# Kernel tuning notes

Hardware: AMD Instinct MI355X
Metric: run time of the kernel (lower is better)

## Reference

```python
import jax, jax.numpy as jnp
import numpy as np

B, DZ, H, DY = 4096, 512, 2048, 10
N_STEPS = 64
SCALE = 0.02  # matches param_ulow/uhigh magnitude


def setup_inputs() -> dict:
    key = jax.random.key(0)
    ks = jax.random.split(key, 6)
    x = jax.random.normal(ks[0], (B, DZ), dtype=jnp.float32)
    A = jax.random.normal(ks[1], (DZ, DZ), dtype=jnp.float32) * SCALE
    W1 = jax.random.normal(ks[2], (H, DZ), dtype=jnp.float32) * SCALE
    b1 = jax.random.normal(ks[3], (H,), dtype=jnp.float32) * SCALE
    W2 = jax.random.normal(ks[4], (DY, H), dtype=jnp.float32) * SCALE
    b2 = jax.random.normal(ks[5], (DY,), dtype=jnp.float32) * SCALE
    return {"x": x, "A": A, "W1": W1, "b1": b1, "W2": W2, "b2": b2,
            "n_steps": N_STEPS}


def reference(x, A, W1, b1, W2, b2, n_steps):
    # Z0 = P @ x with P = I  => Z0 = x
    # dz/dt = einsum('ji,bi->bj', A, z) = z @ A.T ; explicit Euler on [0, 1]
    dt = jnp.float32(1.0 / n_steps)

    def euler_step(z, _):
        return z + dt * (z @ A.T), None

    zT, _ = jax.lax.scan(euler_step, x, None, length=n_steps)  # [B, DZ]
    # Q MLP (n_layers=3): Linear -> ReLU -> Linear
    h = jax.nn.relu(zT @ W1.T + b1)  # [B, H]
    y = h @ W2.T + b2                # [B, DY]
    return y
```

## Files before the change

kernel.cpp:

```cpp
#include <hip/hip_runtime.h>
#include <hip/hip_bf16.h>

#define B_SZ 4096
#define DZ   512
#define H_SZ 2048
#define DY   10

#define C2 0.4921875f
#define C3 0.158935546875f
#define C4 0.037872314453125f
#define C5 ((float)(7624512.0/1073741824.0))
#define C6 ((float)(74974368.0/68719476736.0))

typedef __attribute__((ext_vector_type(8))) __bf16 bf16x8;
typedef __attribute__((ext_vector_type(4))) float  f32x4;
typedef __attribute__((ext_vector_type(8))) unsigned short us8;

__device__ inline unsigned short f2bf(float f) {
    unsigned u = __float_as_uint(f);
    u += 0x7fffu + ((u >> 16) & 1u);
    return (unsigned short)(u >> 16);
}
__device__ inline float bf2f(unsigned short s) {
    return __uint_as_float(((unsigned)s) << 16);
}

__device__ __forceinline__ void gl16(const void* g, void* l) {
    __builtin_amdgcn_global_load_lds(
        (const __attribute__((address_space(1))) unsigned int*)(size_t)g,
        (__attribute__((address_space(3))) unsigned int*)(unsigned)(size_t)l,
        16, 0, 0);
}

union SqSmem {
    struct { unsigned short A[64 * 64]; unsigned short B[64 * 64]; } s;
    float epi[64 * 68];
};

__device__ __forceinline__ void stage64(const unsigned short* __restrict__ src,
                                        unsigned short* lds, int row_base,
                                        int kt, int t) {
    const int w = t >> 6, lane = t & 63;
#pragma unroll
    for (int i = 0; i < 2; ++i) {
        int o = w * 128 + i * 64 + lane;
        int row = o >> 3, cc = (o & 7) ^ (row & 7);
        gl16(&src[(size_t)(row_base + row) * 512 + kt * 64 + cc * 8],
             &lds[(size_t)(w * 128 + i * 64) * 8]);
    }
}

#define MFMA_STEP(acc)                                                        \
    {                                                                         \
        _Pragma("unroll")                                                     \
        for (int ks = 0; ks < 2; ++ks) {                                      \
            bf16x8 af[2], bfr[2];                                             \
            _Pragma("unroll")                                                 \
            for (int i = 0; i < 2; ++i) {                                     \
                int ra = wm + i * 16 + l16, ca = (ks * 4 + quad) ^ (ra & 7);  \
                af[i] = *(const bf16x8*)&sm.s.A[ra * 64 + ca * 8];            \
                int rb = wn + i * 16 + l16, cb = (ks * 4 + quad) ^ (rb & 7);  \
                bfr[i] = *(const bf16x8*)&sm.s.B[rb * 64 + cb * 8];           \
            }                                                                 \
            _Pragma("unroll")                                                 \
            for (int i = 0; i < 2; ++i)                                       \
                _Pragma("unroll")                                             \
                for (int j = 0; j < 2; ++j)                                   \
                    acc[i][j] = __builtin_amdgcn_mfma_f32_16x16x32_bf16(      \
                        af[i], bfr[j], acc[i][j], 0, 0, 0);                   \
        }                                                                     \
    }

#define ACC_TO_EPI(acc)                                                       \
    {                                                                         \
        _Pragma("unroll")                                                     \
        for (int i = 0; i < 2; ++i)                                           \
            _Pragma("unroll")                                                 \
            for (int j = 0; j < 2; ++j)                                       \
                _Pragma("unroll")                                             \
                for (int rr = 0; rr < 4; ++rr)                                \
                    sm.epi[(wm + i * 16 + quad * 4 + rr) * 68 +               \
                           wn + j * 16 + l16] = acc[i][j][rr];                \
        __syncthreads();                                                      \
    }

__device__ inline void gemm64_mfma(const unsigned short* __restrict__ Arows,
                                   const unsigned short* __restrict__ Brows,
                                   int m0, int n0, int t, SqSmem& sm) {
    const int lane = t & 63, w = t >> 6, quad = lane >> 4, l16 = lane & 15;
    const int wm = (w & 1) * 32, wn = (w >> 1) * 32;
    f32x4 acc[2][2];
#pragma unroll
    for (int i = 0; i < 2; ++i)
#pragma unroll
        for (int j = 0; j < 2; ++j) acc[i][j] = (f32x4){0.f, 0.f, 0.f, 0.f};
    for (int kt = 0; kt < 8; ++kt) {
        stage64(Arows, sm.s.A, m0, kt, t);
        stage64(Brows, sm.s.B, n0, kt, t);
        __syncthreads();
        MFMA_STEP(acc)
        __syncthreads();
    }
    ACC_TO_EPI(acc)
}

__device__ inline void gemm64_f32src(const float* __restrict__ Arows,
                                     const float* __restrict__ Bsrc,
                                     int m0, int n0, int t, SqSmem& sm) {
    const int lane = t & 63, w = t >> 6, quad = lane >> 4, l16 = lane & 15;
    const int wm = (w & 1) * 32, wn = (w >> 1) * 32;
    const int r = t >> 2, cq = t & 3;
    f32x4 acc[2][2];
#pragma unroll
    for (int i = 0; i < 2; ++i)
#pragma unroll
        for (int j = 0; j < 2; ++j) acc[i][j] = (f32x4){0.f, 0.f, 0.f, 0.f};
    for (int kt = 0; kt < 8; ++kt) {
        float va[16];
#pragma unroll
        for (int u = 0; u < 4; ++u) {
            float4 f = *(const float4*)&Arows[(size_t)(m0 + r) * 512 + kt * 64 + cq * 16 + u * 4];
            va[u * 4 + 0] = f.x; va[u * 4 + 1] = f.y;
            va[u * 4 + 2] = f.z; va[u * 4 + 3] = f.w;
        }
#pragma unroll
        for (int j2 = 0; j2 < 2; ++j2) {
            us8 h;
#pragma unroll
            for (int j = 0; j < 8; ++j) h[j] = f2bf(va[j2 * 8 + j]);
            int cc = cq * 2 + j2;
            *(us8*)&sm.s.A[r * 64 + (cc ^ (r & 7)) * 8] = h;
        }
#pragma unroll
        for (int u = 0; u < 4; ++u) {
            float4 f = *(const float4*)&Bsrc[(size_t)(kt * 64 + r) * 512 + n0 + cq * 16 + u * 4];
            float vv[4] = {f.x, f.y, f.z, f.w};
#pragma unroll
            for (int j = 0; j < 4; ++j) {
                int n = cq * 16 + u * 4 + j;
                sm.s.B[n * 64 + ((r >> 3) ^ (n & 7)) * 8 + (r & 7)] = f2bf(vv[j]);
            }
        }
        __syncthreads();
        MFMA_STEP(acc)
        __syncthreads();
    }
    ACC_TO_EPI(acc)
}

__device__ inline void epi_out_bf(unsigned short* __restrict__ dst, int m0,
                                  int n0, int t, SqSmem& sm) {
    const int r = t >> 2, cq = t & 3;
    us8 h0, h1;
#pragma unroll
    for (int j = 0; j < 8; ++j) {
        h0[j] = f2bf(sm.epi[r * 68 + cq * 16 + j]);
        h1[j] = f2bf(sm.epi[r * 68 + cq * 16 + 8 + j]);
    }
    *(us8*)&dst[(size_t)(m0 + r) * 512 + n0 + cq * 16]     = h0;
    *(us8*)&dst[(size_t)(m0 + r) * 512 + n0 + cq * 16 + 8] = h1;
}
__device__ inline void epi_out_bfT(unsigned short* __restrict__ dst, int m0,
                                   int n0, int t, SqSmem& sm) {
    const int cf = t >> 2, rq = t & 3;
    us8 o0, o1;
#pragma unroll
    for (int i = 0; i < 8; ++i) {
        o0[i] = f2bf(sm.epi[(rq * 16 + i) * 68 + cf]);
        o1[i] = f2bf(sm.epi[(rq * 16 + 8 + i) * 68 + cf]);
    }
    *(us8*)&dst[(size_t)(n0 + cf) * 512 + m0 + rq * 16]     = o0;
    *(us8*)&dst[(size_t)(n0 + cf) * 512 + m0 + rq * 16 + 8] = o1;
}

__global__ __launch_bounds__(256) void k_s1(
    const float* __restrict__ A, const float* __restrict__ x,
    const float* __restrict__ W1, const float* __restrict__ b2,
    unsigned short* __restrict__ A2_bf, unsigned short* __restrict__ A2T_bf,
    unsigned short* __restrict__ AT_bf, unsigned short* __restrict__ U1_bf,
    unsigned short* __restrict__ x_bf, float* __restrict__ y) {
    __shared__ SqSmem sm;
    const int b = blockIdx.x, t = threadIdx.x;
    const int gid = b * 256 + t;

    const float4* x4 = (const float4*)x;
#pragma unroll
    for (int i = 0; i < 3; ++i) {
        int id = gid + i * 98304;
        if (id < 262144) {
            float4 v0 = x4[(size_t)id * 2], v1 = x4[(size_t)id * 2 + 1];
            us8 o;
            o[0] = f2bf(v0.x); o[1] = f2bf(v0.y); o[2] = f2bf(v0.z); o[3] = f2bf(v0.w);
            o[4] = f2bf(v1.x); o[5] = f2bf(v1.y); o[6] = f2bf(v1.z); o[7] = f2bf(v1.w);
            *(us8*)&x_bf[(size_t)id * 8] = o;
        }
    }
    if (gid < B_SZ * DY) y[gid] = b2[gid % 10];

    if (b < 64) {
        const int m0 = (b >> 3) * 64, n0 = (b & 7) * 64;
        gemm64_f32src(A, A, m0, n0, t, sm);
        epi_out_bf(A2_bf, m0, n0, t, sm);
        epi_out_bfT(A2T_bf, m0, n0, t, sm);
    } else if (b < 128) {
        const int bb = b - 64, m0 = (bb >> 3) * 64, n0 = (bb & 7) * 64;
        const int r = t >> 2, cq = t & 3;
#pragma unroll
        for (int u = 0; u < 4; ++u) {
            float4 f = *(const float4*)&A[(size_t)(m0 + r) * 512 + n0 + cq * 16 + u * 4];
            sm.epi[r * 68 + cq * 16 + u * 4 + 0] = f.x;
            sm.epi[r * 68 + cq * 16 + u * 4 + 1] = f.y;
            sm.epi[r * 68 + cq * 16 + u * 4 + 2] = f.z;
            sm.epi[r * 68 + cq * 16 + u * 4 + 3] = f.w;
        }
        __syncthreads();
        epi_out_bfT(AT_bf, m0, n0, t, sm);
    } else {
        const int bb = b - 128, m0 = (bb >> 3) * 64, n0 = (bb & 7) * 64;
        gemm64_f32src(W1, A, m0, n0, t, sm);
        epi_out_bf(U1_bf, m0, n0, t, sm);
    }
}

__global__ __launch_bounds__(256) void k_s2(
    const unsigned short* __restrict__ A2_bf,
    const unsigned short* __restrict__ A2T_bf,
    const unsigned short* __restrict__ AT_bf,
    const unsigned short* __restrict__ U1_bf,
    unsigned short* __restrict__ A3T_bf, unsigned short* __restrict__ U2_bf,
    unsigned short* __restrict__ U3_bf) {
    __shared__ SqSmem sm;
    const int b = blockIdx.x, t = threadIdx.x;
    if (b < 64) {
        const int m0 = (b >> 3) * 64, n0 = (b & 7) * 64;
        gemm64_mfma(A2_bf, AT_bf, m0, n0, t, sm);
        epi_out_bfT(A3T_bf, m0, n0, t, sm);
    } else if (b < 320) {
        const int bb = b - 64, m0 = (bb >> 3) * 64, n0 = (bb & 7) * 64;
        gemm64_mfma(U1_bf, AT_bf, m0, n0, t, sm);
        epi_out_bf(U2_bf, m0, n0, t, sm);
    } else {
        const int bb = b - 320, m0 = (bb >> 3) * 64, n0 = (bb & 7) * 64;
        gemm64_mfma(U1_bf, A2T_bf, m0, n0, t, sm);
        epi_out_bf(U3_bf, m0, n0, t, sm);
    }
}

__global__ __launch_bounds__(256) void k_s3(
    const float* __restrict__ W1, const unsigned short* __restrict__ U1_bf,
    const unsigned short* __restrict__ U2_bf,
    const unsigned short* __restrict__ U3_bf,
    const unsigned short* __restrict__ A3T_bf,
    unsigned short* __restrict__ w1f) {
    __shared__ SqSmem sm;
    const int b = blockIdx.x, t = threadIdx.x;
    const int m0 = (b >> 3) * 64, n0 = (b & 7) * 64;
    const int lane = t & 63, w = t >> 6, quad = lane >> 4, l16 = lane & 15;
    const int wm = (w & 1) * 32, wn = (w >> 1) * 32;
    f32x4 acc[2][2];
#pragma unroll
    for (int i = 0; i < 2; ++i)
#pragma unroll
        for (int j = 0; j < 2; ++j) acc[i][j] = (f32x4){0.f, 0.f, 0.f, 0.f};
    for (int kt = 0; kt < 8; ++kt) {
        stage64(A3T_bf, sm.s.B, n0, kt, t);
#pragma unroll
        for (int c = 0; c < 2; ++c) {
            int idx = c * 256 + t, row = idx >> 3, cc = idx & 7;
            int ccs = cc ^ (row & 7);
            size_t ga = (size_t)(m0 + row) * 512 + kt * 64 + cc * 8;
            us8 u1 = *(const us8*)&U1_bf[ga];
            us8 u2 = *(const us8*)&U2_bf[ga];
            us8 u3 = *(const us8*)&U3_bf[ga];
            us8 g;
#pragma unroll
            for (int j = 0; j < 8; ++j)
                g[j] = f2bf(C4 * bf2f(u1[j]) + C5 * bf2f(u2[j]) + C6 * bf2f(u3[j]));
            *(us8*)&sm.s.A[row * 64 + ccs * 8] = g;
        }
        __syncthreads();
        MFMA_STEP(acc)
        __syncthreads();
    }
    ACC_TO_EPI(acc)
    const int r = t >> 2, cq = t & 3;
    size_t gbase = (size_t)(m0 + r) * 512 + n0 + cq * 16;
    us8 u1a = *(const us8*)&U1_bf[gbase], u1b = *(const us8*)&U1_bf[gbase + 8];
    us8 u2a = *(const us8*)&U2_bf[gbase], u2b = *(const us8*)&U2_bf[gbase + 8];
    us8 u3a = *(const us8*)&U3_bf[gbase], u3b = *(const us8*)&U3_bf[gbase + 8];
    us8 h0, h1;
#pragma unroll
    for (int u = 0; u < 2; ++u) {
        float4 wv = *(const float4*)&W1[gbase + u * 4];
        float4 wv2 = *(const float4*)&W1[gbase + 8 + u * 4];
#pragma unroll
        for (int j = 0; j < 4; ++j) {
            int e = u * 4 + j;
            float wj = (j == 0 ? wv.x : j == 1 ? wv.y : j == 2 ? wv.z : wv.w);
            float wj2 = (j == 0 ? wv2.x : j == 1 ? wv2.y : j == 2 ? wv2.z : wv2.w);
            h0[e] = f2bf(wj + bf2f(u1a[e]) + C2 * bf2f(u2a[e]) +
                         C3 * bf2f(u3a[e]) + sm.epi[r * 68 + cq * 16 + e]);
            h1[e] = f2bf(wj2 + bf2f(u1b[e]) + C2 * bf2f(u2b[e]) +
                         C3 * bf2f(u3b[e]) + sm.epi[r * 68 + cq * 16 + 8 + e]);
        }
    }
    *(us8*)&w1f[gbase]     = h0;
    *(us8*)&w1f[gbase + 8] = h1;
}

union SmemU {
    struct { unsigned short A[128 * 64]; unsigned short B[128 * 64]; } s;
    struct { unsigned short h[128 * 136]; } e;
};

__global__ __launch_bounds__(256) void mlp_kernel(
    const unsigned short* __restrict__ x_bf,
    const unsigned short* __restrict__ w1f,
    const float* __restrict__ b1, const float* __restrict__ W2,
    float* __restrict__ y) {
    __shared__ SmemU sm;
    const int t    = threadIdx.x;
    const int lane = t & 63, w = t >> 6;
    const int quad = lane >> 4, l16 = lane & 15;
    const int wm = (w & 1) * 64, wn = (w >> 1) * 64;
    const int m0g = blockIdx.x * 128, n0g = blockIdx.y * 128;

    f32x4 acc[4][4];
#pragma unroll
    for (int i = 0; i < 4; ++i)
#pragma unroll
        for (int j = 0; j < 4; ++j) acc[i][j] = (f32x4){0.f, 0.f, 0.f, 0.f};

    for (int kt = 0; kt < 8; ++kt) {
#pragma unroll
        for (int i = 0; i < 4; ++i) {
            int o = w * 256 + i * 64 + lane;
            int row = o >> 3, cc = (o & 7) ^ (row & 7);
            gl16(&x_bf[(size_t)(m0g + row) * 512 + kt * 64 + cc * 8],
                 &sm.s.A[(size_t)(w * 256 + i * 64) * 8]);
        }
#pragma unroll
        for (int i = 0; i < 4; ++i) {
            int o = w * 256 + i * 64 + lane;
            int row = o >> 3, cc = (o & 7) ^ (row & 7);
            gl16(&w1f[(size_t)(n0g + row) * 512 + kt * 64 + cc * 8],
                 &sm.s.B[(size_t)(w * 256 + i * 64) * 8]);
        }
        __syncthreads();
#pragma unroll
        for (int ks = 0; ks < 2; ++ks) {
            bf16x8 af[4], bfr[4];
#pragma unroll
            for (int i = 0; i < 4; ++i) {
                int ra = wm + i * 16 + l16, ca = (ks * 4 + quad) ^ (ra & 7);
                af[i] = *(const bf16x8*)&sm.s.A[ra * 64 + ca * 8];
                int rb = wn + i * 16 + l16, cb = (ks * 4 + quad) ^ (rb & 7);
                bfr[i] = *(const bf16x8*)&sm.s.B[rb * 64 + cb * 8];
            }
#pragma unroll
            for (int i = 0; i < 4; ++i)
// ... 23 lines not shown

    {
        bf16x8 wfrag[4];
#pragma unroll
        for (int kc = 0; kc < 4; ++kc) {
            us8 wb;
            if (l16 < DY) {
                const float* wp = &W2[(size_t)l16 * H_SZ + n0g + kc * 32 + quad * 8];
#pragma unroll
                for (int j = 0; j < 8; ++j) wb[j] = f2bf(wp[j]);
            } else {
#pragma unroll
                for (int j = 0; j < 8; ++j) wb[j] = 0;
            }
            wfrag[kc] = *(bf16x8*)&wb;
        }
#pragma unroll
        for (int hh = 0; hh < 2; ++hh) {
            const int mrow = w * 32 + hh * 16;
            f32x4 ay = (f32x4){0.f, 0.f, 0.f, 0.f};
#pragma unroll
            for (int kc = 0; kc < 4; ++kc) {
                bf16x8 af = *(const bf16x8*)&sm.e.h[(mrow + l16) * 136 +
                                                    kc * 32 + quad * 8];
                ay = __builtin_amdgcn_mfma_f32_16x16x32_bf16(af, wfrag[kc], ay,
                                                             0, 0, 0);
            }
            if (l16 < DY) {
#pragma unroll
                for (int r = 0; r < 4; ++r)
                    atomicAdd(&y[(size_t)(m0g + mrow + quad * 4 + r) * DY + l16],
                              ay[r]);
            }
        }
    }
}

extern "C" void kernel_launch(void* const* d_in, const int* in_sizes, int n_in,
                              void* d_out, int out_size, void* d_ws, size_t ws_size,
                              hipStream_t stream) {
    const float* x  = (const float*)d_in[0];
    const float* A  = (const float*)d_in[1];
    const float* W1 = (const float*)d_in[2];
    const float* b1 = (const float*)d_in[3];
    const float* W2 = (const float*)d_in[4];
    const float* b2 = (const float*)d_in[5];
    float* y = (float*)d_out;

    char* ws = (char*)d_ws;
    const size_t HMB = 512u * 1024, MB = 1u << 20;
    unsigned short* AT_bf  = (unsigned short*)(ws);
    unsigned short* A2_bf  = (unsigned short*)(ws + 1 * HMB);
    unsigned short* A2T_bf = (unsigned short*)(ws + 2 * HMB);
    unsigned short* A3T_bf = (unsigned short*)(ws + 3 * HMB);
    unsigned short* U1_bf  = (unsigned short*)(ws + 2 * MB);
    unsigned short* U2_bf  = (unsigned short*)(ws + 4 * MB);
    unsigned short* U3_bf  = (unsigned short*)(ws + 6 * MB);
    unsigned short* w1f    = (unsigned short*)(ws + 8 * MB);
    unsigned short* x_bf   = (unsigned short*)(ws + 10 * MB);

    k_s1<<<384, 256, 0, stream>>>(A, x, W1, b2, A2_bf, A2T_bf, AT_bf, U1_bf,
                                  x_bf, y);
    k_s2<<<576, 256, 0, stream>>>(A2_bf, A2T_bf, AT_bf, U1_bf, A3T_bf, U2_bf,
                                  U3_bf);
    k_s3<<<256, 256, 0, stream>>>(W1, U1_bf, U2_bf, U3_bf, A3T_bf, w1f);
    mlp_kernel<<<dim3(32, 16), dim3(256), 0, stream>>>(x_bf, w1f, b1, W2, y);
}
```

Before: 135.6 us.

## Restructure matrix-power polynomial to use A^3/A^4 and 128-tile GEMMs

After: 171.6 us. 1.27x slower.

```diff
diff --git a/kernel.cpp b/kernel.cpp
--- a/kernel.cpp
+++ b/kernel.cpp
@@ -36,19 +36,6 @@
     struct { unsigned short A[64 * 64]; unsigned short B[64 * 64]; } s;
     float epi[64 * 68];
 };
-
-__device__ __forceinline__ void stage64(const unsigned short* __restrict__ src,
-                                        unsigned short* lds, int row_base,
-                                        int kt, int t) {
-    const int w = t >> 6, lane = t & 63;
-#pragma unroll
-    for (int i = 0; i < 2; ++i) {
-        int o = w * 128 + i * 64 + lane;
-        int row = o >> 3, cc = (o & 7) ^ (row & 7);
-        gl16(&src[(size_t)(row_base + row) * 512 + kt * 64 + cc * 8],
-             &lds[(size_t)(w * 128 + i * 64) * 8]);
-    }
-}
 
 #define MFMA_STEP(acc)                                                        \
     {                                                                         \
@@ -84,26 +71,6 @@
         __syncthreads();                                                      \
     }
 
-__device__ inline void gemm64_mfma(const unsigned short* __restrict__ Arows,
-                                   const unsigned short* __restrict__ Brows,
-                                   int m0, int n0, int t, SqSmem& sm) {
-    const int lane = t & 63, w = t >> 6, quad = lane >> 4, l16 = lane & 15;
-    const int wm = (w & 1) * 32, wn = (w >> 1) * 32;
-    f32x4 acc[2][2];
-#pragma unroll
-    for (int i = 0; i < 2; ++i)
-#pragma unroll
-        for (int j = 0; j < 2; ++j) acc[i][j] = (f32x4){0.f, 0.f, 0.f, 0.f};
-    for (int kt = 0; kt < 8; ++kt) {
-        stage64(Arows, sm.s.A, m0, kt, t);
-        stage64(Brows, sm.s.B, n0, kt, t);
-        __syncthreads();
-        MFMA_STEP(acc)
-        __syncthreads();
-    }
-    ACC_TO_EPI(acc)
-}
-
 __device__ inline void gemm64_f32src(const float* __restrict__ Arows,
                                      const float* __restrict__ Bsrc,
                                      int m0, int n0, int t, SqSmem& sm) {
@@ -173,27 +140,131 @@
     *(us8*)&dst[(size_t)(n0 + cf) * 512 + m0 + rq * 16 + 8] = o1;
 }
 
+union Smem128 {
+    struct { unsigned short A[128 * 64]; unsigned short B[128 * 64]; } s;
+    float epi[128 * 133];
+};
+
+__device__ __forceinline__ void g128_stage(const unsigned short* __restrict__ Asrc,
+                                           const unsigned short* __restrict__ Bsrc,
+                                           int m0, int n0, int kt, int t,
+                                           Smem128& sm) {
+    const int w = t >> 6, lane = t & 63;
+#pragma unroll
+    for (int i = 0; i < 4; ++i) {
+        int o = w * 256 + i * 64 + lane;
+        int row = o >> 3, cc = (o & 7) ^ (row & 7);
+        gl16(&Asrc[(size_t)(m0 + row) * 512 + kt * 64 + cc * 8],
+             &sm.s.A[(w * 256 + i * 64) * 8]);
+        gl16(&Bsrc[(size_t)(n0 + row) * 512 + kt * 64 + cc * 8],
+             &sm.s.B[(w * 256 + i * 64) * 8]);
+    }
+}
+
+__device__ __forceinline__ void g128_mfma(int t, Smem128& sm, f32x4 acc[4][4]) {
+    const int lane = t & 63, w = t >> 6, quad = lane >> 4, l16 = lane & 15;
+    const int wm = (w & 1) * 64, wn = (w >> 1) * 64;
+#pragma unroll
+    for (int ks = 0; ks < 2; ++ks) {
+        bf16x8 af[4], bfr[4];
+#pragma unroll
+        for (int i = 0; i < 4; ++i) {
+            int ra = wm + i * 16 + l16, ca = (ks * 4 + quad) ^ (ra & 7);
+            af[i] = *(const bf16x8*)&sm.s.A[ra * 64 + ca * 8];
+            int rb = wn + i * 16 + l16, cb = (ks * 4 + quad) ^ (rb & 7);
+            bfr[i] = *(const bf16x8*)&sm.s.B[rb * 64 + cb * 8];
+        }
+#pragma unroll
+        for (int i = 0; i < 4; ++i)
+#pragma unroll
+            for (int j = 0; j < 4; ++j)
+                acc[i][j] = __builtin_amdgcn_mfma_f32_16x16x32_bf16(
+                    af[i], bfr[j], acc[i][j], 0, 0, 0);
+    }
+}
+
+__device__ inline void gemm128(const unsigned short* __restrict__ Asrc,
+                               const unsigned short* __restrict__ Bsrc,
+                               int m0, int n0, int t, Smem128& sm,
+                               f32x4 acc[4][4]) {
+    for (int kt = 0; kt < 8; ++kt) {
+        g128_stage(Asrc, Bsrc, m0, n0, kt, t, sm);
+        __syncthreads();
+        g128_mfma(t, sm, acc);
+        __syncthreads();
+    }
+}
+
+__device__ inline void g128_acc2epi(int t, Smem128& sm, f32x4 acc[4][4]) {
+    const int lane = t & 63, w = t >> 6, quad = lane >> 4, l16 = lane & 15;
+    const int wm = (w & 1) * 64, wn = (w >> 1) * 64;
+#pragma unroll
+    for (int i = 0; i < 4; ++i)
+#pragma unroll
+        for (int j = 0; j < 4; ++j)
+#pragma unroll
+            for (int r = 0; r < 4; ++r)
+                sm.epi[(wm + i * 16 + quad * 4 + r) * 133 + wn + j * 16 + l16] =
+                    acc[i][j][r];
+    __syncthreads();
+}
+
+__device__ inline void g128_out(unsigned short* __restrict__ dst, int m0,
+                                int n0, int t, Smem128& sm) {
+    const int r = t >> 1, hf = t & 1;
+    size_t gb = (size_t)(m0 + r) * 512 + n0 + hf * 64;
+#pragma unroll
+    for (int jc = 0; jc < 8; ++jc) {
+        us8 h;
+#pragma unroll
+        for (int j = 0; j < 8; ++j)
+            h[j] = f2bf(sm.epi[r * 133 + hf * 64 + jc * 8 + j]);
+        *(us8*)&dst[gb + jc * 8] = h;
+    }
+}
+__device__ inline void g128_outT(unsigned short* __restrict__ dst, int m0,
+                                 int n0, int t, Smem128& sm) {
+    const int c = t >> 1, hf = t & 1;
+    size_t gb = (size_t)(n0 + c) * 512 + m0 + hf * 64;
+#pragma unroll
+    for (int jc = 0; jc < 8; ++jc) {
+        us8 h;
+#pragma unroll
+        for (int j = 0; j < 8; ++j)
+            h[j] = f2bf(sm.epi[(hf * 64 + jc * 8 + j) * 133 + c]);
+        *(us8*)&dst[gb + jc * 8] = h;
+    }
+}
+
 __global__ __launch_bounds__(256) void k_s1(
     const float* __restrict__ A, const float* __restrict__ x,
     const float* __restrict__ W1, const float* __restrict__ b2,
     unsigned short* __restrict__ A2_bf, unsigned short* __restrict__ A2T_bf,
-    unsigned short* __restrict__ AT_bf, unsigned short* __restrict__ U1_bf,
-    unsigned short* __restrict__ x_bf, float* __restrict__ y) {
+    unsigned short* __restrict__ AT_bf, unsigned short* __restrict__ x_bf,
+    unsigned short* __restrict__ W1_bf, float* __restrict__ y) {
     __shared__ SqSmem sm;
     const int b = blockIdx.x, t = threadIdx.x;
     const int gid = b * 256 + t;
 
     const float4* x4 = (const float4*)x;
 #pragma unroll
-    for (int i = 0; i < 3; ++i) {
-        int id = gid + i * 98304;
-        if (id < 262144) {
-            float4 v0 = x4[(size_t)id * 2], v1 = x4[(size_t)id * 2 + 1];
-            us8 o;
-            o[0] = f2bf(v0.x); o[1] = f2bf(v0.y); o[2] = f2bf(v0.z); o[3] = f2bf(v0.w);
-            o[4] = f2bf(v1.x); o[5] = f2bf(v1.y); o[6] = f2bf(v1.z); o[7] = f2bf(v1.w);
-            *(us8*)&x_bf[(size_t)id * 8] = o;
-        }
+    for (int i = 0; i < 4; ++i) {
+        int id = gid + i * 65536;
+        float4 v0 = x4[(size_t)id * 2], v1 = x4[(size_t)id * 2 + 1];
+        us8 o;
+        o[0] = f2bf(v0.x); o[1] = f2bf(v0.y); o[2] = f2bf(v0.z); o[3] = f2bf(v0.w);
+        o[4] = f2bf(v1.x); o[5] = f2bf(v1.y); o[6] = f2bf(v1.z); o[7] = f2bf(v1.w);
+        *(us8*)&x_bf[(size_t)id * 8] = o;
+    }
+    const float4* w4 = (const float4*)W1;
+#pragma unroll
+    for (int i = 0; i < 2; ++i) {
+        int id = gid + i * 65536;
+        float4 v0 = w4[(size_t)id * 2], v1 = w4[(size_t)id * 2 + 1];
+        us8 o;
+        o[0] = f2bf(v0.x); o[1] = f2bf(v0.y); o[2] = f2bf(v0.z); o[3] = f2bf(v0.w);
+        o[4] = f2bf(v1.x); o[5] = f2bf(v1.y); o[6] = f2bf(v1.z); o[7] = f2bf(v1.w);
+        *(us8*)&W1_bf[(size_t)id * 8] = o;
     }
     if (gid < B_SZ * DY) y[gid] = b2[gid % 10];
 
@@ -215,97 +286,119 @@
         }
         __syncthreads();
         epi_out_bfT(AT_bf, m0, n0, t, sm);
-    } else {
-        const int bb = b - 128, m0 = (bb >> 3) * 64, n0 = (bb & 7) * 64;
-        gemm64_f32src(W1, A, m0, n0, t, sm);
-        epi_out_bf(U1_bf, m0, n0, t, sm);
     }
 }
 
 __global__ __launch_bounds__(256) void k_s2(
+    const unsigned short* __restrict__ W1_bf,
     const unsigned short* __restrict__ A2_bf,
     const unsigned short* __restrict__ A2T_bf,
     const unsigned short* __restrict__ AT_bf,
-    const unsigned short* __restrict__ U1_bf,
-    unsigned short* __restrict__ A3T_bf, unsigned short* __restrict__ U2_bf,
-    unsigned short* __restrict__ U3_bf) {
-    __shared__ SqSmem sm;
+    unsigned short* __restrict__ A3T_bf, unsigned short* __restrict__ A4T_bf,
+    unsigned short* __restrict__ U1_bf, unsigned short* __restrict__ U2_bf) {
+    __shared__ Smem128 sm;
     const int b = blockIdx.x, t = threadIdx.x;
-    if (b < 64) {
-        const int m0 = (b >> 3) * 64, n0 = (b & 7) * 64;
-        gemm64_mfma(A2_bf, AT_bf, m0, n0, t, sm);
-        epi_out_bfT(A3T_bf, m0, n0, t, sm);
-    } else if (b < 320) {
-        const int bb = b - 64, m0 = (bb >> 3) * 64, n0 = (bb & 7) * 64;
-        gemm64_mfma(U1_bf, AT_bf, m0, n0, t, sm);
-        epi_out_bf(U2_bf, m0, n0, t, sm);
+    f32x4 acc[4][4];
+#pragma unroll
+    for (int i = 0; i < 4; ++i)
+#pragma unroll
+        for (int j = 0; j < 4; ++j) acc[i][j] = (f32x4){0.f, 0.f, 0.f, 0.f};
+
+    if (b < 16) {
+        const int m0 = (b >> 2) * 128, n0 = (b & 3) * 128;
+        gemm128(A2_bf, AT_bf, m0, n0, t, sm, acc);
+        g128_acc2epi(t, sm, acc);
+        g128_outT(A3T_bf, m0, n0, t, sm);
+    } else if (b < 32) {
+        const int bb = b - 16, m0 = (bb >> 2) * 128, n0 = (bb & 3) * 128;
+        gemm128(A2_bf, A2T_bf, m0, n0, t, sm, acc);
+        g128_acc2epi(t, sm, acc);
+        g128_outT(A4T_bf, m0, n0, t, sm);
+    } else if (b < 96) {
+        const int bb = b - 32, m0 = (bb >> 2) * 128, n0 = (bb & 3) * 128;
+        gemm128(W1_bf, AT_bf, m0, n0, t, sm, acc);
+        g128_acc2epi(t, sm, acc);
+        g128_out(U1_bf, m0, n0, t, sm);
     } else {
-        const int bb = b - 320, m0 = (bb >> 3) * 64, n0 = (bb & 7) * 64;
-        gemm64_mfma(U1_bf, A2T_bf, m0, n0, t, sm);
-        epi_out_bf(U3_bf, m0, n0, t, sm);
+        const int bb = b - 96, m0 = (bb >> 2) * 128, n0 = (bb & 3) * 128;
+        gemm128(W1_bf, A2T_bf, m0, n0, t, sm, acc);
+        g128_acc2epi(t, sm, acc);
+        g128_out(U2_bf, m0, n0, t, sm);
     }
 }
 
 __global__ __launch_bounds__(256) void k_s3(
     const float* __restrict__ W1, const unsigned short* __restrict__ U1_bf,
     const unsigned short* __restrict__ U2_bf,
-    const unsigned short* __restrict__ U3_bf,
     const unsigned short* __restrict__ A3T_bf,
+    const unsigned short* __restrict__ A4T_bf,
     unsigned short* __restrict__ w1f) {
-    __shared__ SqSmem sm;
+    __shared__ Smem128 sm;
     const int b = blockIdx.x, t = threadIdx.x;
-    const int m0 = (b >> 3) * 64, n0 = (b & 7) * 64;
-    const int lane = t & 63, w = t >> 6, quad = lane >> 4, l16 = lane & 15;
-    const int wm = (w & 1) * 32, wn = (w >> 1) * 32;
-    f32x4 acc[2][2];
-#pragma unroll
-    for (int i = 0; i < 2; ++i)
-#pragma unroll
-        for (int j = 0; j < 2; ++j) acc[i][j] = (f32x4){0.f, 0.f, 0.f, 0.f};
-    for (int kt = 0; kt < 8; ++kt) {
-        stage64(A3T_bf, sm.s.B, n0, kt, t);
-#pragma unroll
-        for (int c = 0; c < 2; ++c) {
-            int idx = c * 256 + t, row = idx >> 3, cc = idx & 7;
-            int ccs = cc ^ (row & 7);
-            size_t ga = (size_t)(m0 + row) * 512 + kt * 64 + cc * 8;
-            us8 u1 = *(const us8*)&U1_bf[ga];
-            us8 u2 = *(const us8*)&U2_bf[ga];
-            us8 u3 = *(const us8*)&U3_bf[ga];
-            us8 g;
-#pragma unroll
-            for (int j = 0; j < 8; ++j)
-                g[j] = f2bf(C4 * bf2f(u1[j]) + C5 * bf2f(u2[j]) + C6 * bf2f(u3[j]));
-            *(us8*)&sm.s.A[row * 64 + ccs * 8] = g;
-        }
-        __syncthreads();
-        MFMA_STEP(acc)
-        __syncthreads();
-    }
-    ACC_TO_EPI(acc)
-    const int r = t >> 2, cq = t & 3;
-    size_t gbase = (size_t)(m0 + r) * 512 + n0 + cq * 16;
-    us8 u1a = *(const us8*)&U1_bf[gbase], u1b = *(const us8*)&U1_bf[gbase + 8];
-    us8 u2a = *(const us8*)&U2_bf[gbase], u2b = *(const us8*)&U2_bf[gbase + 8];
-    us8 u3a = *(const us8*)&U3_bf[gbase], u3b = *(const us8*)&U3_bf[gbase + 8];
-    us8 h0, h1;
-#pragma unroll
-    for (int u = 0; u < 2; ++u) {
-        float4 wv = *(const float4*)&W1[gbase + u * 4];
-        float4 wv2 = *(const float4*)&W1[gbase + 8 + u * 4];
-#pragma unroll
-        for (int j = 0; j < 4; ++j) {
-            int e = u * 4 + j;
-            float wj = (j == 0 ? wv.x : j == 1 ? wv.y : j == 2 ? wv.z : wv.w);
-            float wj2 = (j == 0 ? wv2.x : j == 1 ? wv2.y : j == 2 ? wv2.z : wv2.w);
-            h0[e] = f2bf(wj + bf2f(u1a[e]) + C2 * bf2f(u2a[e]) +
-                         C3 * bf2f(u3a[e]) + sm.epi[r * 68 + cq * 16 + e]);
-            h1[e] = f2bf(wj2 + bf2f(u1b[e]) + C2 * bf2f(u2b[e]) +
-                         C3 * bf2f(u3b[e]) + sm.epi[r * 68 + cq * 16 + 8 + e]);
-        }
-    }
-    *(us8*)&w1f[gbase]     = h0;
-    *(us8*)&w1f[gbase + 8] = h1;
+    const int m0 = (b >> 2) * 128, n0 = (b & 3) * 128;
+    const int w = t >> 6, lane = t & 63;
+    f32x4 acc[4][4];
+#pragma unroll
+    for (int i = 0; i < 4; ++i)
+#pragma unroll
+        for (int j = 0; j < 4; ++j) acc[i][j] = (f32x4){0.f, 0.f, 0.f, 0.f};
+
+    for (int pass = 0; pass < 2; ++pass) {
+        const unsigned short* __restrict__ Bt = pass ? A4T_bf : A3T_bf;
+        for (int kt = 0; kt < 8; ++kt) {
+#pragma unroll
+            for (int i = 0; i < 4; ++i) {
+                int o = w * 256 + i * 64 + lane;
+                int row = o >> 3, cc = (o & 7) ^ (row & 7);
+                gl16(&Bt[(size_t)(n0 + row) * 512 + kt * 64 + cc * 8],
+                     &sm.s.B[(w * 256 + i * 64) * 8]);
+            }
+#pragma unroll
+            for (int c = 0; c < 4; ++c) {
+                int idx = c * 256 + t, row = idx >> 3, cc = idx & 7;
+                int ccs = cc ^ (row & 7);
+                size_t ga = (size_t)(m0 + row) * 512 + kt * 64 + cc * 8;
+                us8 g;
+                if (pass == 0) {
+                    us8 u1 = *(const us8*)&U1_bf[ga];
+                    us8 u2 = *(const us8*)&U2_bf[ga];
+                    float4 wa = *(const float4*)&W1[ga];
+                    float4 wb = *(const float4*)&W1[ga + 4];
+                    float wf[8] = {wa.x, wa.y, wa.z, wa.w, wb.x, wb.y, wb.z, wb.w};
+#pragma unroll
+                    for (int j = 0; j < 8; ++j)
+                        g[j] = f2bf(C3 * wf[j] + C4 * bf2f(u1[j]) +
+                                    C5 * bf2f(u2[j]));
+                } else {
+                    us8 u2 = *(const us8*)&U2_bf[ga];
+#pragma unroll
+                    for (int j = 0; j < 8; ++j) g[j] = f2bf(C6 * bf2f(u2[j]));
+                }
+                *(us8*)&sm.s.A[row * 64 + ccs * 8] = g;
+            }
+            __syncthreads();
+            g128_mfma(t, sm, acc);
+            __syncthreads();
+        }
+    }
+    g128_acc2epi(t, sm, acc);
+
+    const int r = t >> 1, hf = t & 1;
+    size_t gb = (size_t)(m0 + r) * 512 + n0 + hf * 64;
+#pragma unroll
+    for (int jc = 0; jc < 8; ++jc) {
+        us8 u1 = *(const us8*)&U1_bf[gb + jc * 8];
+        us8 u2 = *(const us8*)&U2_bf[gb + jc * 8];
+        float4 wa = *(const float4*)&W1[gb + jc * 8];
+        float4 wb = *(const float4*)&W1[gb + jc * 8 + 4];
+        float wf[8] = {wa.x, wa.y, wa.z, wa.w, wb.x, wb.y, wb.z, wb.w};
+        us8 h;
+#pragma unroll
+        for (int j = 0; j < 8; ++j)
+            h[j] = f2bf(wf[j] + bf2f(u1[j]) + C2 * bf2f(u2[j]) +
+                        sm.epi[r * 133 + hf * 64 + jc * 8 + j]);
+        *(us8*)&w1f[gb + jc * 8] = h;
+    }
 }
 
 union SmemU {
@@ -436,16 +529,17 @@
     unsigned short* A2_bf  = (unsigned short*)(ws + 1 * HMB);
     unsigned short* A2T_bf = (unsigned short*)(ws + 2 * HMB);
     unsigned short* A3T_bf = (unsigned short*)(ws + 3 * HMB);
-    unsigned short* U1_bf  = (unsigned short*)(ws + 2 * MB);
-    unsigned short* U2_bf  = (unsigned short*)(ws + 4 * MB);
-    unsigned short* U3_bf  = (unsigned short*)(ws + 6 * MB);
-    unsigned short* w1f    = (unsigned short*)(ws + 8 * MB);
-    unsigned short* x_bf   = (unsigned short*)(ws + 10 * MB);
-
-    k_s1<<<384, 256, 0, stream>>>(A, x, W1, b2, A2_bf, A2T_bf, AT_bf, U1_bf,
-                                  x_bf, y);
-    k_s2<<<576, 256, 0, stream>>>(A2_bf, A2T_bf, AT_bf, U1_bf, A3T_bf, U2_bf,
-                                  U3_bf);
-    k_s3<<<256, 256, 0, stream>>>(W1, U1_bf, U2_bf, U3_bf, A3T_bf, w1f);
+    unsigned short* A4T_bf = (unsigned short*)(ws + 4 * HMB);
+    unsigned short* U1_bf  = (unsigned short*)(ws + 5 * HMB);
+    unsigned short* U2_bf  = (unsigned short*)(ws + 5 * HMB + 2 * MB);
+    unsigned short* w1f    = (unsigned short*)(ws + 5 * HMB + 4 * MB);
+    unsigned short* x_bf   = (unsigned short*)(ws + 5 * HMB + 6 * MB);
+    unsigned short* W1_bf  = (unsigned short*)(ws + 5 * HMB + 10 * MB);
+
+    k_s1<<<256, 256, 0, stream>>>(A, x, W1, b2, A2_bf, A2T_bf, AT_bf, x_bf,
+                                  W1_bf, y);
+    k_s2<<<160, 256, 0, stream>>>(W1_bf, A2_bf, A2T_bf, AT_bf, A3T_bf, A4T_bf,
+                                  U1_bf, U2_bf);
+    k_s3<<<64, 256, 0, stream>>>(W1, U1_bf, U2_bf, A3T_bf, A4T_bf, w1f);
     mlp_kernel<<<dim3(32, 16), dim3(256), 0, stream>>>(x_bf, w1f, b1, W2, y);
 }
```

## Build Euler polynomial in A-space before folding it into W1

Applied to the files above, without the earlier changes.

New measurement: 142.1 us. +4.8%, slower.

```diff
diff --git a/kernel.cpp b/kernel.cpp
--- a/kernel.cpp
+++ b/kernel.cpp
@@ -177,25 +177,11 @@
     const float* __restrict__ A, const float* __restrict__ x,
     const float* __restrict__ W1, const float* __restrict__ b2,
     unsigned short* __restrict__ A2_bf, unsigned short* __restrict__ A2T_bf,
-    unsigned short* __restrict__ AT_bf, unsigned short* __restrict__ U1_bf,
-    unsigned short* __restrict__ x_bf, float* __restrict__ y) {
+    unsigned short* __restrict__ AT_bf, unsigned short* __restrict__ A_bf,
+    unsigned short* __restrict__ x_bf, unsigned short* __restrict__ W1_bf,
+    float* __restrict__ y) {
     __shared__ SqSmem sm;
     const int b = blockIdx.x, t = threadIdx.x;
-    const int gid = b * 256 + t;
-
-    const float4* x4 = (const float4*)x;
-#pragma unroll
-    for (int i = 0; i < 3; ++i) {
-        int id = gid + i * 98304;
-        if (id < 262144) {
-            float4 v0 = x4[(size_t)id * 2], v1 = x4[(size_t)id * 2 + 1];
-            us8 o;
-            o[0] = f2bf(v0.x); o[1] = f2bf(v0.y); o[2] = f2bf(v0.z); o[3] = f2bf(v0.w);
-            o[4] = f2bf(v1.x); o[5] = f2bf(v1.y); o[6] = f2bf(v1.z); o[7] = f2bf(v1.w);
-            *(us8*)&x_bf[(size_t)id * 8] = o;
-        }
-    }
-    if (gid < B_SZ * DY) y[gid] = b2[gid % 10];
 
     if (b < 64) {
         const int m0 = (b >> 3) * 64, n0 = (b & 7) * 64;
@@ -216,42 +202,61 @@
         __syncthreads();
         epi_out_bfT(AT_bf, m0, n0, t, sm);
     } else {
-        const int bb = b - 128, m0 = (bb >> 3) * 64, n0 = (bb & 7) * 64;
-        gemm64_f32src(W1, A, m0, n0, t, sm);
-        epi_out_bf(U1_bf, m0, n0, t, sm);
+        const int gid = (b - 128) * 256 + t;
+        const float4* x4 = (const float4*)x;
+#pragma unroll
+        for (int i = 0; i < 8; ++i) {
+            int id = gid + i * 32768;
+            float4 v0 = x4[(size_t)id * 2], v1 = x4[(size_t)id * 2 + 1];
+            us8 o;
+            o[0] = f2bf(v0.x); o[1] = f2bf(v0.y); o[2] = f2bf(v0.z); o[3] = f2bf(v0.w);
+            o[4] = f2bf(v1.x); o[5] = f2bf(v1.y); o[6] = f2bf(v1.z); o[7] = f2bf(v1.w);
+            *(us8*)&x_bf[(size_t)id * 8] = o;
+        }
+        const float4* w4 = (const float4*)W1;
+#pragma unroll
+        for (int i = 0; i < 4; ++i) {
+            int id = gid + i * 32768;
+            float4 v0 = w4[(size_t)id * 2], v1 = w4[(size_t)id * 2 + 1];
+            us8 o;
+            o[0] = f2bf(v0.x); o[1] = f2bf(v0.y); o[2] = f2bf(v0.z); o[3] = f2bf(v0.w);
+            o[4] = f2bf(v1.x); o[5] = f2bf(v1.y); o[6] = f2bf(v1.z); o[7] = f2bf(v1.w);
+            *(us8*)&W1_bf[(size_t)id * 8] = o;
+        }
+        {
+            const float4* a4 = (const float4*)A;
+            float4 v0 = a4[(size_t)gid * 2], v1 = a4[(size_t)gid * 2 + 1];
+            us8 o;
+            o[0] = f2bf(v0.x); o[1] = f2bf(v0.y); o[2] = f2bf(v0.z); o[3] = f2bf(v0.w);
+            o[4] = f2bf(v1.x); o[5] = f2bf(v1.y); o[6] = f2bf(v1.z); o[7] = f2bf(v1.w);
+            *(us8*)&A_bf[(size_t)gid * 8] = o;
+        }
+#pragma unroll
+        for (int i = 0; i < 2; ++i) {
+            int id = gid + i * 32768;
+            if (id < B_SZ * DY) y[id] = b2[id % 10];
+        }
     }
 }
 
 __global__ __launch_bounds__(256) void k_s2(
     const unsigned short* __restrict__ A2_bf,
     const unsigned short* __restrict__ A2T_bf,
-    const unsigned short* __restrict__ AT_bf,
-    const unsigned short* __restrict__ U1_bf,
-    unsigned short* __restrict__ A3T_bf, unsigned short* __restrict__ U2_bf,
-    unsigned short* __restrict__ U3_bf) {
+    unsigned short* __restrict__ A4T_bf) {
     __shared__ SqSmem sm;
     const int b = blockIdx.x, t = threadIdx.x;
-    if (b < 64) {
-        const int m0 = (b >> 3) * 64, n0 = (b & 7) * 64;
-        gemm64_mfma(A2_bf, AT_bf, m0, n0, t, sm);
-        epi_out_bfT(A3T_bf, m0, n0, t, sm);
-    } else if (b < 320) {
-        const int bb = b - 64, m0 = (bb >> 3) * 64, n0 = (bb & 7) * 64;
-        gemm64_mfma(U1_bf, AT_bf, m0, n0, t, sm);
-        epi_out_bf(U2_bf, m0, n0, t, sm);
-    } else {
-        const int bb = b - 320, m0 = (bb >> 3) * 64, n0 = (bb & 7) * 64;
-        gemm64_mfma(U1_bf, A2T_bf, m0, n0, t, sm);
-        epi_out_bf(U3_bf, m0, n0, t, sm);
-    }
+    const int m0 = (b >> 3) * 64, n0 = (b & 7) * 64;
+    gemm64_mfma(A2_bf, A2T_bf, m0, n0, t, sm);
+    epi_out_bfT(A4T_bf, m0, n0, t, sm);
 }
 
 __global__ __launch_bounds__(256) void k_s3(
-    const float* __restrict__ W1, const unsigned short* __restrict__ U1_bf,
-    const unsigned short* __restrict__ U2_bf,
-    const unsigned short* __restrict__ U3_bf,
-    const unsigned short* __restrict__ A3T_bf,
-    unsigned short* __restrict__ w1f) {
+    const unsigned short* __restrict__ A_bf,
+    const unsigned short* __restrict__ A2_bf,
+    const unsigned short* __restrict__ A2T_bf,
+    const unsigned short* __restrict__ A4T_bf,
+    const unsigned short* __restrict__ AT_bf,
+    unsigned short* __restrict__ QpT_bf) {
     __shared__ SqSmem sm;
     const int b = blockIdx.x, t = threadIdx.x;
     const int m0 = (b >> 3) * 64, n0 = (b & 7) * 64;
@@ -262,50 +267,73 @@
     for (int i = 0; i < 2; ++i)
 #pragma unroll
         for (int j = 0; j < 2; ++j) acc[i][j] = (f32x4){0.f, 0.f, 0.f, 0.f};
-    for (int kt = 0; kt < 8; ++kt) {
-        stage64(A3T_bf, sm.s.B, n0, kt, t);
-#pragma unroll
-        for (int c = 0; c < 2; ++c) {
-            int idx = c * 256 + t, row = idx >> 3, cc = idx & 7;
-            int ccs = cc ^ (row & 7);
-            size_t ga = (size_t)(m0 + row) * 512 + kt * 64 + cc * 8;
-            us8 u1 = *(const us8*)&U1_bf[ga];
-            us8 u2 = *(const us8*)&U2_bf[ga];
-            us8 u3 = *(const us8*)&U3_bf[ga];
-            us8 g;
-#pragma unroll
-            for (int j = 0; j < 8; ++j)
-                g[j] = f2bf(C4 * bf2f(u1[j]) + C5 * bf2f(u2[j]) + C6 * bf2f(u3[j]));
-            *(us8*)&sm.s.A[row * 64 + ccs * 8] = g;
-        }
-        __syncthreads();
-        MFMA_STEP(acc)
-        __syncthreads();
+
+#pragma unroll
+    for (int pass = 0; pass < 2; ++pass) {
+        const unsigned short* __restrict__ Bt = pass ? A4T_bf : A2T_bf;
+        const float cA  = pass ? C5 : C3;
+        const float cA2 = pass ? C6 : C4;
+        for (int kt = 0; kt < 8; ++kt) {
+            stage64(Bt, sm.s.B, n0, kt, t);
+#pragma unroll
+            for (int c = 0; c < 2; ++c) {
+                int idx = c * 256 + t, row = idx >> 3, cc = idx & 7;
+                int ccs = cc ^ (row & 7);
+                size_t ga = (size_t)(m0 + row) * 512 + kt * 64 + cc * 8;
+                us8 a  = *(const us8*)&A_bf[ga];
+                us8 a2 = *(const us8*)&A2_bf[ga];
+                us8 g;
+#pragma unroll
+                for (int j = 0; j < 8; ++j)
+                    g[j] = f2bf(cA * bf2f(a[j]) + cA2 * bf2f(a2[j]));
+                *(us8*)&sm.s.A[row * 64 + ccs * 8] = g;
+            }
+            __syncthreads();
+            MFMA_STEP(acc)
+            __syncthreads();
+        }
     }
     ACC_TO_EPI(acc)
+
+    const int cf = t >> 2, rq = t & 3;
+    size_t gb = (size_t)(n0 + cf) * 512 + m0 + rq * 16;
+    us8 at0  = *(const us8*)&AT_bf[gb],  at1  = *(const us8*)&AT_bf[gb + 8];
+    us8 a2t0 = *(const us8*)&A2T_bf[gb], a2t1 = *(const us8*)&A2T_bf[gb + 8];
+    us8 o0, o1;
+#pragma unroll
+    for (int i = 0; i < 8; ++i) {
+        o0[i] = f2bf(bf2f(at0[i]) + C2 * bf2f(a2t0[i]) +
+                     sm.epi[(rq * 16 + i) * 68 + cf]);
+        o1[i] = f2bf(bf2f(at1[i]) + C2 * bf2f(a2t1[i]) +
+                     sm.epi[(rq * 16 + 8 + i) * 68 + cf]);
+    }
+    *(us8*)&QpT_bf[gb]     = o0;
+    *(us8*)&QpT_bf[gb + 8] = o1;
+}
+
+__global__ __launch_bounds__(256) void k_s4(
+    const unsigned short* __restrict__ W1_bf,
+    const unsigned short* __restrict__ QpT_bf,
+    const float* __restrict__ W1, unsigned short* __restrict__ w1f) {
+    __shared__ SqSmem sm;
+    const int b = blockIdx.x, t = threadIdx.x;
+    const int m0 = (b >> 3) * 64, n0 = (b & 7) * 64;
+    gemm64_mfma(W1_bf, QpT_bf, m0, n0, t, sm);
+
     const int r = t >> 2, cq = t & 3;
-    size_t gbase = (size_t)(m0 + r) * 512 + n0 + cq * 16;
-    us8 u1a = *(const us8*)&U1_bf[gbase], u1b = *(const us8*)&U1_bf[gbase + 8];
-    us8 u2a = *(const us8*)&U2_bf[gbase], u2b = *(const us8*)&U2_bf[gbase + 8];
-    us8 u3a = *(const us8*)&U3_bf[gbase], u3b = *(const us8*)&U3_bf[gbase + 8];
+    size_t gb = (size_t)(m0 + r) * 512 + n0 + cq * 16;
+    float4 wa = *(const float4*)&W1[gb],      wbv = *(const float4*)&W1[gb + 4];
+    float4 wc = *(const float4*)&W1[gb + 8],  wd  = *(const float4*)&W1[gb + 12];
+    float wf[16] = {wa.x, wa.y, wa.z, wa.w, wbv.x, wbv.y, wbv.z, wbv.w,
+                    wc.x, wc.y, wc.z, wc.w, wd.x,  wd.y,  wd.z,  wd.w};
     us8 h0, h1;
 #pragma unroll
-    for (int u = 0; u < 2; ++u) {
-        float4 wv = *(const float4*)&W1[gbase + u * 4];
-        float4 wv2 = *(const float4*)&W1[gbase + 8 + u * 4];
-#pragma unroll
-        for (int j = 0; j < 4; ++j) {
-            int e = u * 4 + j;
-            float wj = (j == 0 ? wv.x : j == 1 ? wv.y : j == 2 ? wv.z : wv.w);
-            float wj2 = (j == 0 ? wv2.x : j == 1 ? wv2.y : j == 2 ? wv2.z : wv2.w);
-            h0[e] = f2bf(wj + bf2f(u1a[e]) + C2 * bf2f(u2a[e]) +
-                         C3 * bf2f(u3a[e]) + sm.epi[r * 68 + cq * 16 + e]);
-            h1[e] = f2bf(wj2 + bf2f(u1b[e]) + C2 * bf2f(u2b[e]) +
-                         C3 * bf2f(u3b[e]) + sm.epi[r * 68 + cq * 16 + 8 + e]);
-        }
-    }
-    *(us8*)&w1f[gbase]     = h0;
-    *(us8*)&w1f[gbase + 8] = h1;
+    for (int j = 0; j < 8; ++j) {
+        h0[j] = f2bf(wf[j]     + sm.epi[r * 68 + cq * 16 + j]);
+        h1[j] = f2bf(wf[8 + j] + sm.epi[r * 68 + cq * 16 + 8 + j]);
+    }
+    *(us8*)&w1f[gb]     = h0;
+    *(us8*)&w1f[gb + 8] = h1;
 }
 
 union SmemU {
@@ -435,17 +463,17 @@
     unsigned short* AT_bf  = (unsigned short*)(ws);
     unsigned short* A2_bf  = (unsigned short*)(ws + 1 * HMB);
     unsigned short* A2T_bf = (unsigned short*)(ws + 2 * HMB);
-    unsigned short* A3T_bf = (unsigned short*)(ws + 3 * HMB);
-    unsigned short* U1_bf  = (unsigned short*)(ws + 2 * MB);
-    unsigned short* U2_bf  = (unsigned short*)(ws + 4 * MB);
-    unsigned short* U3_bf  = (unsigned short*)(ws + 6 * MB);
-    unsigned short* w1f    = (unsigned short*)(ws + 8 * MB);
-    unsigned short* x_bf   = (unsigned short*)(ws + 10 * MB);
-
-    k_s1<<<384, 256, 0, stream>>>(A, x, W1, b2, A2_bf, A2T_bf, AT_bf, U1_bf,
-                                  x_bf, y);
-    k_s2<<<576, 256, 0, stream>>>(A2_bf, A2T_bf, AT_bf, U1_bf, A3T_bf, U2_bf,
-                                  U3_bf);
-    k_s3<<<256, 256, 0, stream>>>(W1, U1_bf, U2_bf, U3_bf, A3T_bf, w1f);
+    unsigned short* A4T_bf = (unsigned short*)(ws + 3 * HMB);
+    unsigned short* A_bf   = (unsigned short*)(ws + 4 * HMB);
+    unsigned short* QpT_bf = (unsigned short*)(ws + 5 * HMB);
+    unsigned short* w1f    = (unsigned short*)(ws + 3 * MB);
+    unsigned short* W1_bf  = (unsigned short*)(ws + 5 * MB);
+    unsigned short* x_bf   = (unsigned short*)(ws + 7 * MB);
+
+    k_s1<<<256, 256, 0, stream>>>(A, x, W1, b2, A2_bf, A2T_bf, AT_bf, A_bf,
+                                  x_bf, W1_bf, y);
+    k_s2<<<64, 256, 0, stream>>>(A2_bf, A2T_bf, A4T_bf);
+    k_s3<<<64, 256, 0, stream>>>(A_bf, A2_bf, A2T_bf, A4T_bf, AT_bf, QpT_bf);
+    k_s4<<<256, 256, 0, stream>>>(W1_bf, QpT_bf, W1, w1f);
     mlp_kernel<<<dim3(32, 16), dim3(256), 0, stream>>>(x_bf, w1f, b1, W2, y);
 }
```

## Restructure Taylor-series weight fold to use A^2/A^4 and drop fp32 W1·A GEMM

Applied to the files above, without the earlier changes.

Measured after the change: 140.7 us. +3.8%, slower.

```diff
diff --git a/kernel.cpp b/kernel.cpp
--- a/kernel.cpp
+++ b/kernel.cpp
@@ -177,25 +177,10 @@
     const float* __restrict__ A, const float* __restrict__ x,
     const float* __restrict__ W1, const float* __restrict__ b2,
     unsigned short* __restrict__ A2_bf, unsigned short* __restrict__ A2T_bf,
-    unsigned short* __restrict__ AT_bf, unsigned short* __restrict__ U1_bf,
-    unsigned short* __restrict__ x_bf, float* __restrict__ y) {
+    unsigned short* __restrict__ AT_bf, unsigned short* __restrict__ x_bf,
+    unsigned short* __restrict__ W1_bf, float* __restrict__ y) {
     __shared__ SqSmem sm;
     const int b = blockIdx.x, t = threadIdx.x;
-    const int gid = b * 256 + t;
-
-    const float4* x4 = (const float4*)x;
-#pragma unroll
-    for (int i = 0; i < 3; ++i) {
-        int id = gid + i * 98304;
-        if (id < 262144) {
-            float4 v0 = x4[(size_t)id * 2], v1 = x4[(size_t)id * 2 + 1];
-            us8 o;
-            o[0] = f2bf(v0.x); o[1] = f2bf(v0.y); o[2] = f2bf(v0.z); o[3] = f2bf(v0.w);
-            o[4] = f2bf(v1.x); o[5] = f2bf(v1.y); o[6] = f2bf(v1.z); o[7] = f2bf(v1.w);
-            *(us8*)&x_bf[(size_t)id * 8] = o;
-        }
-    }
-    if (gid < B_SZ * DY) y[gid] = b2[gid % 10];
 
     if (b < 64) {
         const int m0 = (b >> 3) * 64, n0 = (b & 7) * 64;
@@ -216,41 +201,64 @@
         __syncthreads();
         epi_out_bfT(AT_bf, m0, n0, t, sm);
     } else {
-        const int bb = b - 128, m0 = (bb >> 3) * 64, n0 = (bb & 7) * 64;
-        gemm64_f32src(W1, A, m0, n0, t, sm);
-        epi_out_bf(U1_bf, m0, n0, t, sm);
+        const int gid = (b - 128) * 256 + t;
+        const float4* x4 = (const float4*)x;
+#pragma unroll
+        for (int i = 0; i < 8; ++i) {
+            int id = gid + i * 32768;
+            float4 v0 = x4[(size_t)id * 2], v1 = x4[(size_t)id * 2 + 1];
+            us8 o;
+            o[0] = f2bf(v0.x); o[1] = f2bf(v0.y); o[2] = f2bf(v0.z); o[3] = f2bf(v0.w);
+            o[4] = f2bf(v1.x); o[5] = f2bf(v1.y); o[6] = f2bf(v1.z); o[7] = f2bf(v1.w);
+            *(us8*)&x_bf[(size_t)id * 8] = o;
+        }
+        const float4* w4 = (const float4*)W1;
+#pragma unroll
+        for (int i = 0; i < 4; ++i) {
+            int id = gid + i * 32768;
+            float4 v0 = w4[(size_t)id * 2], v1 = w4[(size_t)id * 2 + 1];
+            us8 o;
+            o[0] = f2bf(v0.x); o[1] = f2bf(v0.y); o[2] = f2bf(v0.z); o[3] = f2bf(v0.w);
+            o[4] = f2bf(v1.x); o[5] = f2bf(v1.y); o[6] = f2bf(v1.z); o[7] = f2bf(v1.w);
+            *(us8*)&W1_bf[(size_t)id * 8] = o;
+        }
+#pragma unroll
+        for (int i = 0; i < 2; ++i) {
+            int id = gid + i * 32768;
+            if (id < B_SZ * DY) y[id] = b2[id % 10];
+        }
     }
 }
 
 __global__ __launch_bounds__(256) void k_s2(
+    const unsigned short* __restrict__ W1_bf,
     const unsigned short* __restrict__ A2_bf,
     const unsigned short* __restrict__ A2T_bf,
     const unsigned short* __restrict__ AT_bf,
-    const unsigned short* __restrict__ U1_bf,
-    unsigned short* __restrict__ A3T_bf, unsigned short* __restrict__ U2_bf,
-    unsigned short* __restrict__ U3_bf) {
+    unsigned short* __restrict__ A4T_bf, unsigned short* __restrict__ U1_bf,
+    unsigned short* __restrict__ U2_bf) {
     __shared__ SqSmem sm;
     const int b = blockIdx.x, t = threadIdx.x;
     if (b < 64) {
         const int m0 = (b >> 3) * 64, n0 = (b & 7) * 64;
-        gemm64_mfma(A2_bf, AT_bf, m0, n0, t, sm);
-        epi_out_bfT(A3T_bf, m0, n0, t, sm);
+        gemm64_mfma(A2T_bf, A2_bf, m0, n0, t, sm);
+        epi_out_bf(A4T_bf, m0, n0, t, sm);
     } else if (b < 320) {
         const int bb = b - 64, m0 = (bb >> 3) * 64, n0 = (bb & 7) * 64;
-        gemm64_mfma(U1_bf, AT_bf, m0, n0, t, sm);
-        epi_out_bf(U2_bf, m0, n0, t, sm);
+        gemm64_mfma(W1_bf, AT_bf, m0, n0, t, sm);
+        epi_out_bf(U1_bf, m0, n0, t, sm);
     } else {
         const int bb = b - 320, m0 = (bb >> 3) * 64, n0 = (bb & 7) * 64;
-        gemm64_mfma(U1_bf, A2T_bf, m0, n0, t, sm);
-        epi_out_bf(U3_bf, m0, n0, t, sm);
+        gemm64_mfma(W1_bf, A2T_bf, m0, n0, t, sm);
+        epi_out_bf(U2_bf, m0, n0, t, sm);
     }
 }
 
 __global__ __launch_bounds__(256) void k_s3(
     const float* __restrict__ W1, const unsigned short* __restrict__ U1_bf,
     const unsigned short* __restrict__ U2_bf,
-    const unsigned short* __restrict__ U3_bf,
-    const unsigned short* __restrict__ A3T_bf,
+    const unsigned short* __restrict__ A2T_bf,
+    const unsigned short* __restrict__ A4T_bf,
     unsigned short* __restrict__ w1f) {
     __shared__ SqSmem sm;
     const int b = blockIdx.x, t = threadIdx.x;
@@ -262,47 +270,49 @@
     for (int i = 0; i < 2; ++i)
 #pragma unroll
         for (int j = 0; j < 2; ++j) acc[i][j] = (f32x4){0.f, 0.f, 0.f, 0.f};
-    for (int kt = 0; kt < 8; ++kt) {
-        stage64(A3T_bf, sm.s.B, n0, kt, t);
-#pragma unroll
-        for (int c = 0; c < 2; ++c) {
-            int idx = c * 256 + t, row = idx >> 3, cc = idx & 7;
-            int ccs = cc ^ (row & 7);
-            size_t ga = (size_t)(m0 + row) * 512 + kt * 64 + cc * 8;
-            us8 u1 = *(const us8*)&U1_bf[ga];
-            us8 u2 = *(const us8*)&U2_bf[ga];
-            us8 u3 = *(const us8*)&U3_bf[ga];
-            us8 g;
-#pragma unroll
-            for (int j = 0; j < 8; ++j)
-                g[j] = f2bf(C4 * bf2f(u1[j]) + C5 * bf2f(u2[j]) + C6 * bf2f(u3[j]));
-            *(us8*)&sm.s.A[row * 64 + ccs * 8] = g;
-        }
-        __syncthreads();
-        MFMA_STEP(acc)
-        __syncthreads();
+
+#pragma unroll
+    for (int pass = 0; pass < 2; ++pass) {
+        const unsigned short* __restrict__ Bt = pass ? A4T_bf : A2T_bf;
+        const float c1c = pass ? C5 : C3;
+        const float c2c = pass ? C6 : C4;
+        for (int kt = 0; kt < 8; ++kt) {
+            stage64(Bt, sm.s.B, n0, kt, t);
+#pragma unroll
+            for (int c = 0; c < 2; ++c) {
+                int idx = c * 256 + t, row = idx >> 3, cc = idx & 7;
+                int ccs = cc ^ (row & 7);
+                size_t ga = (size_t)(m0 + row) * 512 + kt * 64 + cc * 8;
+                us8 u1 = *(const us8*)&U1_bf[ga];
+                us8 u2 = *(const us8*)&U2_bf[ga];
+                us8 g;
+#pragma unroll
+                for (int j = 0; j < 8; ++j)
+                    g[j] = f2bf(c1c * bf2f(u1[j]) + c2c * bf2f(u2[j]));
+                *(us8*)&sm.s.A[row * 64 + ccs * 8] = g;
+            }
+            __syncthreads();
+            MFMA_STEP(acc)
+            __syncthreads();
+        }
     }
     ACC_TO_EPI(acc)
+
     const int r = t >> 2, cq = t & 3;
     size_t gbase = (size_t)(m0 + r) * 512 + n0 + cq * 16;
     us8 u1a = *(const us8*)&U1_bf[gbase], u1b = *(const us8*)&U1_bf[gbase + 8];
     us8 u2a = *(const us8*)&U2_bf[gbase], u2b = *(const us8*)&U2_bf[gbase + 8];
-    us8 u3a = *(const us8*)&U3_bf[gbase], u3b = *(const us8*)&U3_bf[gbase + 8];
+    float4 wa = *(const float4*)&W1[gbase],      wbv = *(const float4*)&W1[gbase + 4];
+    float4 wc = *(const float4*)&W1[gbase + 8],  wd  = *(const float4*)&W1[gbase + 12];
+    float wf[16] = {wa.x, wa.y, wa.z, wa.w, wbv.x, wbv.y, wbv.z, wbv.w,
+                    wc.x, wc.y, wc.z, wc.w, wd.x,  wd.y,  wd.z,  wd.w};
     us8 h0, h1;
 #pragma unroll
-    for (int u = 0; u < 2; ++u) {
-        float4 wv = *(const float4*)&W1[gbase + u * 4];
-        float4 wv2 = *(const float4*)&W1[gbase + 8 + u * 4];
-#pragma unroll
-        for (int j = 0; j < 4; ++j) {
-            int e = u * 4 + j;
-            float wj = (j == 0 ? wv.x : j == 1 ? wv.y : j == 2 ? wv.z : wv.w);
-            float wj2 = (j == 0 ? wv2.x : j == 1 ? wv2.y : j == 2 ? wv2.z : wv2.w);
-            h0[e] = f2bf(wj + bf2f(u1a[e]) + C2 * bf2f(u2a[e]) +
-                         C3 * bf2f(u3a[e]) + sm.epi[r * 68 + cq * 16 + e]);
-            h1[e] = f2bf(wj2 + bf2f(u1b[e]) + C2 * bf2f(u2b[e]) +
-                         C3 * bf2f(u3b[e]) + sm.epi[r * 68 + cq * 16 + 8 + e]);
-        }
+    for (int j = 0; j < 8; ++j) {
+        h0[j] = f2bf(wf[j] + bf2f(u1a[j]) + C2 * bf2f(u2a[j]) +
+                     sm.epi[r * 68 + cq * 16 + j]);
+        h1[j] = f2bf(wf[8 + j] + bf2f(u1b[j]) + C2 * bf2f(u2b[j]) +
+                     sm.epi[r * 68 + cq * 16 + 8 + j]);
     }
     *(us8*)&w1f[gbase]     = h0;
     *(us8*)&w1f[gbase + 8] = h1;
@@ -435,17 +445,17 @@
     unsigned short* AT_bf  = (unsigned short*)(ws);
     unsigned short* A2_bf  = (unsigned short*)(ws + 1 * HMB);
     unsigned short* A2T_bf = (unsigned short*)(ws + 2 * HMB);
-    unsigned short* A3T_bf = (unsigned short*)(ws + 3 * HMB);
+    unsigned short* A4T_bf = (unsigned short*)(ws + 3 * HMB);
     unsigned short* U1_bf  = (unsigned short*)(ws + 2 * MB);
     unsigned short* U2_bf  = (unsigned short*)(ws + 4 * MB);
-    unsigned short* U3_bf  = (unsigned short*)(ws + 6 * MB);
-    unsigned short* w1f    = (unsigned short*)(ws + 8 * MB);
+    unsigned short* w1f    = (unsigned short*)(ws + 6 * MB);
+    unsigned short* W1_bf  = (unsigned short*)(ws + 8 * MB);
     unsigned short* x_bf   = (unsigned short*)(ws + 10 * MB);
 
-    k_s1<<<384, 256, 0, stream>>>(A, x, W1, b2, A2_bf, A2T_bf, AT_bf, U1_bf,
-                                  x_bf, y);
-    k_s2<<<576, 256, 0, stream>>>(A2_bf, A2T_bf, AT_bf, U1_bf, A3T_bf, U2_bf,
-                                  U3_bf);
-    k_s3<<<256, 256, 0, stream>>>(W1, U1_bf, U2_bf, U3_bf, A3T_bf, w1f);
+    k_s1<<<256, 256, 0, stream>>>(A, x, W1, b2, A2_bf, A2T_bf, AT_bf, x_bf,
+                                  W1_bf, y);
+    k_s2<<<576, 256, 0, stream>>>(W1_bf, A2_bf, A2T_bf, AT_bf, A4T_bf, U1_bf,
+                                  U2_bf);
+    k_s3<<<256, 256, 0, stream>>>(W1, U1_bf, U2_bf, A2T_bf, A4T_bf, w1f);
     mlp_kernel<<<dim3(32, 16), dim3(256), 0, stream>>>(x_bf, w1f, b1, W2, y);
 }
```
